# Optimization experiments

Hardware: AMD Instinct MI355X
Metric: run time of the kernel (lower is better)

## Reference

```python
import jax, jax.numpy as jnp
import numpy as np

B, N, M, D = 16, 1024, 4096, 256

def setup_inputs() -> dict:
    key = jax.random.key(0)
    k1, k2 = jax.random.split(key)
    encode = jax.random.normal(k1, (B, N, D), dtype=jnp.float32)
    # Codebook initialized uniform(-1/M, 1/M) in the torch module; use normal-scaled
    # values of comparable magnitude for a non-degenerate test.
    templat = jax.random.uniform(k2, (M, D), dtype=jnp.float32, minval=-1.0 / M, maxval=1.0 / M)
    return {"encode": encode, "templat": templat}

def reference(encode, templat):
    # eval-mode forward: match(encode, sample=False), detach='encode'
    enc = jax.lax.stop_gradient(encode)
    # squared-L2 distance via the expansion used in the source
    # dist[b,n,m] = |e|^2 - 2 e.t + |t|^2
    e_sq = jnp.sum(enc * enc, axis=-1, keepdims=True)        # (B,N,1)
    t_sq = jnp.sum(templat * templat, axis=-1)                # (M,)
    cross = jnp.einsum('bnd,md->bnm', enc, templat)           # (B,N,M)
    logits = -(e_sq - 2.0 * cross + t_sq)                     # (B,N,M)
    # zsoft = softmax(logits) computed in the module but only zidx/quant returned
    zidx = jnp.argmax(logits, axis=-1)                        # (B,N) int
    quant = templat[zidx]                                     # (B,N,D) gather
    return quant, zidx
```

## Files before the change

### kernel.cpp

```cpp
#include <hip/hip_runtime.h>


typedef _Float16 half8 __attribute__((ext_vector_type(8)));
typedef float f32x4 __attribute__((ext_vector_type(4)));

constexpr int B_ = 16, N_ = 1024, M_ = 4096, D_ = 256;
constexpr int ROWS = B_ * N_;
constexpr int BR = 128;
constexpr int BC = 128;
constexpr int NCT = 4;
constexpr int CS = 8;
constexpr int CPB = BC * NCT;
constexpr int KC = 32;
constexpr int LDH = 40;
constexpr int NPART = CS * 2;
constexpr float TSCALE = 131072.0f;
constexpr float INV2 = 1.52587890625e-05f;

__global__ void split_kernel(const float* __restrict__ E, const float* __restrict__ T,
                             _Float16* __restrict__ Ehi, _Float16* __restrict__ Elo,
                             _Float16* __restrict__ Thi, _Float16* __restrict__ Tlo) {
    int idx = blockIdx.x * blockDim.x + threadIdx.x;
    int row = idx >> 5;
    int c8 = (idx & 31) * 8;
    if (row >= ROWS + M_) return;
    const float* src;
    _Float16 *hi, *lo;
    size_t off;
    float scale;
    if (row < ROWS) {
        off = (size_t)row * D_ + c8;
        src = E + off; hi = Ehi; lo = Elo; scale = 1.0f;
    } else {
        off = (size_t)(row - ROWS) * D_ + c8;
        src = T + off; hi = Thi; lo = Tlo; scale = TSCALE;
    }
    float x[8];
    *reinterpret_cast<float4*>(&x[0]) = *reinterpret_cast<const float4*>(src);
    *reinterpret_cast<float4*>(&x[4]) = *reinterpret_cast<const float4*>(src + 4);
    half8 h, l;
    #pragma unroll
    for (int j = 0; j < 8; j++) {
        float xs = x[j] * scale;
        _Float16 hh = (_Float16)xs;
        h[j] = hh;
        l[j] = (_Float16)(xs - (float)hh);
    }
    *reinterpret_cast<half8*>(hi + off) = h;
    *reinterpret_cast<half8*>(lo + off) = l;
}

__global__ void rowsq_kernel(const float* __restrict__ E, const float* __restrict__ T,
                             float* __restrict__ esq, float* __restrict__ tsq) {
    int gt = blockIdx.x * blockDim.x + threadIdx.x;
    int row = gt >> 4;
    int l = gt & 15;
    if (row >= ROWS + M_) return;
    const float* src = (row < ROWS) ? (E + (size_t)row * D_)
                                    : (T + (size_t)(row - ROWS) * D_);
    const float* p = src + (l >> 3) * 128 + (l & 7);
    float r = __fmul_rn(p[0], p[0]);
    #pragma unroll
    for (int i = 1; i < 16; i++) {
        float x = p[8 * i];
        r = __fadd_rn(r, __fmul_rn(x, x));
    }
    float u = __fadd_rn(r, __shfl_xor(r, 1, 64));
    float v = __fadd_rn(u, __shfl_xor(u, 2, 64));
    float w = __fadd_rn(v, __shfl_xor(v, 4, 64));
    float s = __fadd_rn(w, __shfl_xor(w, 8, 64));
    if (l == 0) {
        if (row < ROWS) esq[row] = s;
        else            tsq[row - ROWS] = s;
    }
}

__global__ __launch_bounds__(256) void score_kernel(
    const _Float16* __restrict__ Ehi_g, const _Float16* __restrict__ Elo_g,
    const _Float16* __restrict__ Thi_g, const _Float16* __restrict__ Tlo_g,
    const float* __restrict__ esq, const float* __restrict__ tsq,
    float2* __restrict__ part) {
    __shared__ _Float16 Ehi[BR][LDH];
    __shared__ _Float16 Elo[BR][LDH];
    __shared__ _Float16 Thi[BC][LDH];
    __shared__ _Float16 Tlo[BC][LDH];

    const int tid = threadIdx.x;
    const int w  = tid >> 6;
    const int l  = tid & 63;
    const int wr = w >> 1;
    const int wc = w & 1;
    const int q  = l >> 4;
    const int cl = l & 15;
    const int row0 = blockIdx.x * BR;
    const int cs = blockIdx.y;
    const int colB = cs * CPB;

    const int srow  = tid >> 1;
    const int skoff = (tid & 1) * 16;

    float er[16];
    #pragma unroll
    for (int fr = 0; fr < 4; fr++)
        #pragma unroll
        for (int rg = 0; rg < 4; rg++)
            er[fr * 4 + rg] = esq[row0 + wr * 64 + fr * 16 + q * 4 + rg];

    float best[16];
    int   bidx[16];
    #pragma unroll
    for (int i = 0; i < 16; i++) { best[i] = 3.4e38f; bidx[i] = 0; }

    for (int ct = 0; ct < NCT; ct++) {
        const int col0 = colB + ct * BC;
        f32x4 acc[4][4];
        #pragma unroll
        for (int i = 0; i < 4; i++)
            #pragma unroll
            for (int j = 0; j < 4; j++)
                acc[i][j] = (f32x4){0.f, 0.f, 0.f, 0.f};

        for (int kc = 0; kc < D_; kc += KC) {
            __syncthreads();
            {
                const size_t eo = (size_t)(row0 + srow) * D_ + kc + skoff;
                half8 eh0 = *reinterpret_cast<const half8*>(Ehi_g + eo);
                half8 eh1 = *reinterpret_cast<const half8*>(Ehi_g + eo + 8);
                half8 el0 = *reinterpret_cast<const half8*>(Elo_g + eo);
                half8 el1 = *reinterpret_cast<const half8*>(Elo_g + eo + 8);
                const size_t to = (size_t)(col0 + srow) * D_ + kc + skoff;
                half8 th0 = *reinterpret_cast<const half8*>(Thi_g + to);
                half8 th1 = *reinterpret_cast<const half8*>(Thi_g + to + 8);
                half8 tl0 = *reinterpret_cast<const half8*>(Tlo_g + to);
                half8 tl1 = *reinterpret_cast<const half8*>(Tlo_g + to + 8);
                *reinterpret_cast<half8*>(&Ehi[srow][skoff])     = eh0;
                *reinterpret_cast<half8*>(&Ehi[srow][skoff + 8]) = eh1;
                *reinterpret_cast<half8*>(&Elo[srow][skoff])     = el0;
                *reinterpret_cast<half8*>(&Elo[srow][skoff + 8]) = el1;
                *reinterpret_cast<half8*>(&Thi[srow][skoff])     = th0;
                *reinterpret_cast<half8*>(&Thi[srow][skoff + 8]) = th1;
                *reinterpret_cast<half8*>(&Tlo[srow][skoff])     = tl0;
                *reinterpret_cast<half8*>(&Tlo[srow][skoff + 8]) = tl1;
            }
            __syncthreads();

            half8 ah[4], bh[4], tmp[4];
            #pragma unroll
            for (int f = 0; f < 4; f++)
                ah[f] = *reinterpret_cast<const half8*>(&Ehi[wr * 64 + f * 16 + cl][q * 8]);
            #pragma unroll
            for (int f = 0; f < 4; f++)
                bh[f] = *reinterpret_cast<const half8*>(&Thi[wc * 64 + f * 16 + cl][q * 8]);
            #pragma unroll
            for (int i = 0; i < 4; i++)
                #pragma unroll
                for (int j = 0; j < 4; j++)
                    acc[i][j] = __builtin_amdgcn_mfma_f32_16x16x32_f16(ah[i], bh[j], acc[i][j], 0, 0, 0);
            #pragma unroll
            for (int f = 0; f < 4; f++)
                tmp[f] = *reinterpret_cast<const half8*>(&Tlo[wc * 64 + f * 16 + cl][q * 8]);
            #pragma unroll
            for (int i = 0; i < 4; i++)
                #pragma unroll
                for (int j = 0; j < 4; j++)
                    acc[i][j] = __builtin_amdgcn_mfma_f32_16x16x32_f16(ah[i], tmp[j], acc[i][j], 0, 0, 0);
            #pragma unroll
            for (int f = 0; f < 4; f++)
                tmp[f] = *reinterpret_cast<const half8*>(&Elo[wr * 64 + f * 16 + cl][q * 8]);
            #pragma unroll
            for (int i = 0; i < 4; i++)
                #pragma unroll
                for (int j = 0; j < 4; j++)
                    acc[i][j] = __builtin_amdgcn_mfma_f32_16x16x32_f16(tmp[i], bh[j], acc[i][j], 0, 0, 0);
        }

        #pragma unroll
        for (int fc = 0; fc < 4; fc++) {
            const int col = col0 + wc * 64 + fc * 16 + cl;
            const float tc = tsq[col];
            #pragma unroll
            for (int fr = 0; fr < 4; fr++)
                #pragma unroll
                for (int rg = 0; rg < 4; rg++) {
                    const float c2 = acc[fr][fc][rg] * INV2;
                    const float d1 = __fsub_rn(er[fr * 4 + rg], c2);
                    const float d2 = __fadd_rn(d1, tc);
                    const int s = fr * 4 + rg;
                    if (d2 < best[s]) { best[s] = d2; bidx[s] = col; }
                }
        }
    }

    #pragma unroll
    for (int s = 0; s < 16; s++) {
        float v = best[s]; int i = bidx[s];
        #pragma unroll
        for (int off = 1; off < 16; off <<= 1) {
            float ov = __shfl_xor(v, off, 64);
            int   oi = __shfl_xor(i, off, 64);
            if (ov < v || (ov == v && oi < i)) { v = ov; i = oi; }
        }
        if (cl == 0) {
            const int row = row0 + wr * 64 + (s >> 2) * 16 + q * 4 + (s & 3);
            part[(size_t)row * NPART + cs * 2 + wc] = make_float2(v, __int_as_float(i));
        }
    }
}

__global__ void gather_kernel(const float* __restrict__ T, const float2* __restrict__ part,
                              float* __restrict__ quant, float* __restrict__ zout) {
    int gt = blockIdx.x * blockDim.x + threadIdx.x;
    int w = gt >> 6, lane = gt & 63;
    if (w >= ROWS) return;
    float2 p = part[(size_t)w * NPART];
    float v = p.x; int idx = __float_as_int(p.y);
    #pragma unroll
    for (int c = 1; c < NPART; c++) {
        float2 q = part[(size_t)w * NPART + c];
        int qi = __float_as_int(q.y);
        if (q.x < v || (q.x == v && qi < idx)) { v = q.x; idx = qi; }
    }
    float4 t = *reinterpret_cast<const float4*>(T + (size_t)idx * D_ + lane * 4);
    *reinterpret_cast<float4*>(quant + (size_t)w * D_ + lane * 4) = t;
    if (lane == 0) zout[w] = (float)idx;
}

extern "C" void kernel_launch(void* const* d_in, const int* in_sizes, int n_in,
                              void* d_out, int out_size, void* d_ws, size_t ws_size,
                              hipStream_t stream) {
    const float* E = (const float*)d_in[0];
    const float* T = (const float*)d_in[1];
    float* quant = (float*)d_out;
    float* zout  = quant + (size_t)ROWS * D_;

    float* esq   = (float*)d_ws;
    float* tsq   = esq + ROWS;
    float2* part = (float2*)(tsq + M_);
    _Float16* Ehi = (_Float16*)(part + (size_t)ROWS * NPART);
    _Float16* Elo = Ehi + (size_t)ROWS * D_;
    _Float16* Thi = Elo + (size_t)ROWS * D_;
    _Float16* Tlo = Thi + (size_t)M_ * D_;

    hipLaunchKernelGGL(split_kernel, dim3((ROWS + M_) * 32 / 256), dim3(256), 0, stream,
                       E, T, Ehi, Elo, Thi, Tlo);
    hipLaunchKernelGGL(rowsq_kernel, dim3((ROWS + M_) * 16 / 256), dim3(256), 0, stream, E, T, esq, tsq);
    hipLaunchKernelGGL(score_kernel, dim3(ROWS / BR, CS), dim3(256), 0, stream,
                       Ehi, Elo, Thi, Tlo, esq, tsq, part);
    hipLaunchKernelGGL(gather_kernel, dim3(ROWS * 64 / 256), dim3(256), 0, stream, T, part, quant, zout);
}
```

Measured before the change: 154.6 us.

## Double-buffer LDS tiles with register prefetch and flatten chunk loop

Flattens the column-tile and K-chunk loops into a single loop over chunks and double-buffers the shared-memory tiles. The next chunk's global loads are issued into registers right after the barrier so they overlap the MFMA work, which also removes one barrier per chunk. LDS row padding changes from 40 to 36 halves, so LDS accesses are split into 8-byte pieces to keep them aligned, which likely targets bank conflicts. The costs are doubled LDS, extra live registers for the prefetch and more, narrower LDS instructions.

```diff
diff --git a/kernel.cpp b/kernel.cpp
--- a/kernel.cpp
+++ b/kernel.cpp
@@ -1,6 +1,7 @@
 #include <hip/hip_runtime.h>
 
 
+typedef _Float16 half4 __attribute__((ext_vector_type(4)));
 typedef _Float16 half8 __attribute__((ext_vector_type(8)));
 typedef float f32x4 __attribute__((ext_vector_type(4)));
 
@@ -12,10 +13,23 @@
 constexpr int CS = 8;
 constexpr int CPB = BC * NCT;
 constexpr int KC = 32;
-constexpr int LDH = 40;
+constexpr int NCH = NCT * (D_ / KC);
+constexpr int LDH = 36;
 constexpr int NPART = CS * 2;
 constexpr float TSCALE = 131072.0f;
 constexpr float INV2 = 1.52587890625e-05f;
+
+__device__ inline void st8(_Float16* p, half8 v) {
+    half4 a = {v[0], v[1], v[2], v[3]};
+    half4 b = {v[4], v[5], v[6], v[7]};
+    *reinterpret_cast<half4*>(p) = a;
+    *reinterpret_cast<half4*>(p + 4) = b;
+}
+__device__ inline half8 ld8(const _Float16* p) {
+    half4 a = *reinterpret_cast<const half4*>(p);
+    half4 b = *reinterpret_cast<const half4*>(p + 4);
+    return (half8){a[0], a[1], a[2], a[3], b[0], b[1], b[2], b[3]};
+}
 
 __global__ void split_kernel(const float* __restrict__ E, const float* __restrict__ T,
                              _Float16* __restrict__ Ehi, _Float16* __restrict__ Elo,
@@ -80,10 +94,10 @@
     const _Float16* __restrict__ Thi_g, const _Float16* __restrict__ Tlo_g,
     const float* __restrict__ esq, const float* __restrict__ tsq,
     float2* __restrict__ part) {
-    __shared__ _Float16 Ehi[BR][LDH];
-    __shared__ _Float16 Elo[BR][LDH];
-    __shared__ _Float16 Thi[BC][LDH];
-    __shared__ _Float16 Tlo[BC][LDH];
+    __shared__ _Float16 Eh[2][BR][LDH];
+    __shared__ _Float16 El[2][BR][LDH];
+    __shared__ _Float16 Th[2][BC][LDH];
+    __shared__ _Float16 Tl[2][BC][LDH];
 
     const int tid = threadIdx.x;
     const int w  = tid >> 6;
@@ -111,84 +125,90 @@
     #pragma unroll
     for (int i = 0; i < 16; i++) { best[i] = 3.4e38f; bidx[i] = 0; }
 
-    for (int ct = 0; ct < NCT; ct++) {
-        const int col0 = colB + ct * BC;
-        f32x4 acc[4][4];
-        #pragma unroll
-        for (int i = 0; i < 4; i++)
-            #pragma unroll
-            for (int j = 0; j < 4; j++)
-                acc[i][j] = (f32x4){0.f, 0.f, 0.f, 0.f};
-
-        for (int kc = 0; kc < D_; kc += KC) {
-            __syncthreads();
-            {
-                const size_t eo = (size_t)(row0 + srow) * D_ + kc + skoff;
-                half8 eh0 = *reinterpret_cast<const half8*>(Ehi_g + eo);
-                half8 eh1 = *reinterpret_cast<const half8*>(Ehi_g + eo + 8);
-                half8 el0 = *reinterpret_cast<const half8*>(Elo_g + eo);
-                half8 el1 = *reinterpret_cast<const half8*>(Elo_g + eo + 8);
-                const size_t to = (size_t)(col0 + srow) * D_ + kc + skoff;
-                half8 th0 = *reinterpret_cast<const half8*>(Thi_g + to);
-                half8 th1 = *reinterpret_cast<const half8*>(Thi_g + to + 8);
-                half8 tl0 = *reinterpret_cast<const half8*>(Tlo_g + to);
-                half8 tl1 = *reinterpret_cast<const half8*>(Tlo_g + to + 8);
-                *reinterpret_cast<half8*>(&Ehi[srow][skoff])     = eh0;
-                *reinterpret_cast<half8*>(&Ehi[srow][skoff + 8]) = eh1;
-                *reinterpret_cast<half8*>(&Elo[srow][skoff])     = el0;
-                *reinterpret_cast<half8*>(&Elo[srow][skoff + 8]) = el1;
-                *reinterpret_cast<half8*>(&Thi[srow][skoff])     = th0;
-                *reinterpret_cast<half8*>(&Thi[srow][skoff + 8]) = th1;
-                *reinterpret_cast<half8*>(&Tlo[srow][skoff])     = tl0;
-                *reinterpret_cast<half8*>(&Tlo[srow][skoff + 8]) = tl1;
-            }
-            __syncthreads();
-
-            half8 ah[4], bh[4], tmp[4];
-            #pragma unroll
-            for (int f = 0; f < 4; f++)
-                ah[f] = *reinterpret_cast<const half8*>(&Ehi[wr * 64 + f * 16 + cl][q * 8]);
-            #pragma unroll
-            for (int f = 0; f < 4; f++)
-                bh[f] = *reinterpret_cast<const half8*>(&Thi[wc * 64 + f * 16 + cl][q * 8]);
+    half8 rE0, rE1, rF0, rF1, rG0, rG1, rH0, rH1;
+    const size_t eo_base = (size_t)(row0 + srow) * D_ + skoff;
+    #define LOADREGS(ch)                                                        \
+        {                                                                       \
+            const int ct_ = (ch) >> 3, kc_ = ((ch) & 7) * KC;                   \
+            const size_t eo = eo_base + kc_;                                    \
+            const size_t to = (size_t)(colB + ct_ * BC + srow) * D_ + kc_ + skoff; \
+            rE0 = *reinterpret_cast<const half8*>(Ehi_g + eo);                  \
+            rE1 = *reinterpret_cast<const half8*>(Ehi_g + eo + 8);              \
+            rF0 = *reinterpret_cast<const half8*>(Elo_g + eo);                  \
+            rF1 = *reinterpret_cast<const half8*>(Elo_g + eo + 8);              \
+            rG0 = *reinterpret_cast<const half8*>(Thi_g + to);                  \
+            rG1 = *reinterpret_cast<const half8*>(Thi_g + to + 8);              \
+            rH0 = *reinterpret_cast<const half8*>(Tlo_g + to);                  \
+            rH1 = *reinterpret_cast<const half8*>(Tlo_g + to + 8);              \
+        }
+
+    LOADREGS(0);
+    f32x4 acc[4][4];
+    int buf = 0;
+
+    for (int ch = 0; ch < NCH; ++ch) {
+        if ((ch & 7) == 0) {
             #pragma unroll
             for (int i = 0; i < 4; i++)
                 #pragma unroll
                 for (int j = 0; j < 4; j++)
-                    acc[i][j] = __builtin_amdgcn_mfma_f32_16x16x32_f16(ah[i], bh[j], acc[i][j], 0, 0, 0);
-            #pragma unroll
-            for (int f = 0; f < 4; f++)
-                tmp[f] = *reinterpret_cast<const half8*>(&Tlo[wc * 64 + f * 16 + cl][q * 8]);
-            #pragma unroll
-            for (int i = 0; i < 4; i++)
+                    acc[i][j] = (f32x4){0.f, 0.f, 0.f, 0.f};
+        }
+        st8(&Eh[buf][srow][skoff], rE0); st8(&Eh[buf][srow][skoff + 8], rE1);
+        st8(&El[buf][srow][skoff], rF0); st8(&El[buf][srow][skoff + 8], rF1);
+        st8(&Th[buf][srow][skoff], rG0); st8(&Th[buf][srow][skoff + 8], rG1);
+        st8(&Tl[buf][srow][skoff], rH0); st8(&Tl[buf][srow][skoff + 8], rH1);
+        __syncthreads();
+        if (ch < NCH - 1) LOADREGS(ch + 1);
+
+        half8 ah[4], bh[4], tmp[4];
+        #pragma unroll
+        for (int f = 0; f < 4; f++)
+            ah[f] = ld8(&Eh[buf][wr * 64 + f * 16 + cl][q * 8]);
+        #pragma unroll
+        for (int f = 0; f < 4; f++)
+            bh[f] = ld8(&Th[buf][wc * 64 + f * 16 + cl][q * 8]);
+        #pragma unroll
+        for (int i = 0; i < 4; i++)
+            #pragma unroll
+            for (int j = 0; j < 4; j++)
+                acc[i][j] = __builtin_amdgcn_mfma_f32_16x16x32_f16(ah[i], bh[j], acc[i][j], 0, 0, 0);
+        #pragma unroll
+        for (int f = 0; f < 4; f++)
+            tmp[f] = ld8(&Tl[buf][wc * 64 + f * 16 + cl][q * 8]);
+        #pragma unroll
+        for (int i = 0; i < 4; i++)
+            #pragma unroll
+            for (int j = 0; j < 4; j++)
+                acc[i][j] = __builtin_amdgcn_mfma_f32_16x16x32_f16(ah[i], tmp[j], acc[i][j], 0, 0, 0);
+        #pragma unroll
+        for (int f = 0; f < 4; f++)
+            tmp[f] = ld8(&El[buf][wr * 64 + f * 16 + cl][q * 8]);
+        #pragma unroll
+        for (int i = 0; i < 4; i++)
+            #pragma unroll
+            for (int j = 0; j < 4; j++)
+                acc[i][j] = __builtin_amdgcn_mfma_f32_16x16x32_f16(tmp[i], bh[j], acc[i][j], 0, 0, 0);
+
+        if ((ch & 7) == 7) {
+            const int col0 = colB + (ch >> 3) * BC;
+            #pragma unroll
+            for (int fc = 0; fc < 4; fc++) {
+                const int col = col0 + wc * 64 + fc * 16 + cl;
+                const float tc = tsq[col];
                 #pragma unroll
-                for (int j = 0; j < 4; j++)
-                    acc[i][j] = __builtin_amdgcn_mfma_f32_16x16x32_f16(ah[i], tmp[j], acc[i][j], 0, 0, 0);
-            #pragma unroll
-            for (int f = 0; f < 4; f++)
-                tmp[f] = *reinterpret_cast<const half8*>(&Elo[wr * 64 + f * 16 + cl][q * 8]);
-            #pragma unroll
-            for (int i = 0; i < 4; i++)
-                #pragma unroll
-                for (int j = 0; j < 4; j++)
-                    acc[i][j] = __builtin_amdgcn_mfma_f32_16x16x32_f16(tmp[i], bh[j], acc[i][j], 0, 0, 0);
-        }
-
-        #pragma unroll
-        for (int fc = 0; fc < 4; fc++) {
-            const int col = col0 + wc * 64 + fc * 16 + cl;
-            const float tc = tsq[col];
-            #pragma unroll
-            for (int fr = 0; fr < 4; fr++)
-                #pragma unroll
-                for (int rg = 0; rg < 4; rg++) {
-                    const float c2 = acc[fr][fc][rg] * INV2;
-                    const float d1 = __fsub_rn(er[fr * 4 + rg], c2);
-                    const float d2 = __fadd_rn(d1, tc);
-                    const int s = fr * 4 + rg;
-                    if (d2 < best[s]) { best[s] = d2; bidx[s] = col; }
-                }
-        }
+                for (int fr = 0; fr < 4; fr++)
+                    #pragma unroll
+                    for (int rg = 0; rg < 4; rg++) {
+                        const float c2 = acc[fr][fc][rg] * INV2;
+                        const float d1 = __fsub_rn(er[fr * 4 + rg], c2);
+                        const float d2 = __fadd_rn(d1, tc);
+                        const int s = fr * 4 + rg;
+                        if (d2 < best[s]) { best[s] = d2; bidx[s] = col; }
+                    }
+            }
+        }
+        buf ^= 1;
     }
 
     #pragma unroll
```

After: 231.9 us. 1.5x slower.

## Stage score-kernel tiles with direct global-to-LDS loads and flatten chunk loop

Applied to the files above, without the earlier changes.

Replaces the register-staged global loads and LDS stores in the score kernel with global_load_lds direct-to-LDS transfers of 16 bytes per lane. The LDS row stride drops from 40 to 32 halves so each wave's rows are contiguous, as the intrinsic requires. The column-tile and k-chunk loops are merged into one flat loop, with accumulators reset and the argmin epilogue run at tile boundaries. This removes the VGPR round-trip and the separate ds_write instructions, but the unpadded stride may bring back LDS bank conflicts on the MFMA fragment reads, and there is still no double buffering.

```diff
diff --git a/kernel.cpp b/kernel.cpp
--- a/kernel.cpp
+++ b/kernel.cpp
@@ -12,10 +12,17 @@
 constexpr int CS = 8;
 constexpr int CPB = BC * NCT;
 constexpr int KC = 32;
-constexpr int LDH = 40;
+constexpr int NCH = NCT * (D_ / KC);
+constexpr int LDH = 32;
 constexpr int NPART = CS * 2;
 constexpr float TSCALE = 131072.0f;
 constexpr float INV2 = 1.52587890625e-05f;
+
+__device__ __forceinline__ void gload16(const _Float16* g, _Float16* l) {
+    __builtin_amdgcn_global_load_lds(
+        (const __attribute__((address_space(1))) void*)g,
+        (__attribute__((address_space(3))) void*)l, 16, 0, 0);
+}
 
 __global__ void split_kernel(const float* __restrict__ E, const float* __restrict__ T,
                              _Float16* __restrict__ Ehi, _Float16* __restrict__ Elo,
@@ -80,10 +87,10 @@
     const _Float16* __restrict__ Thi_g, const _Float16* __restrict__ Tlo_g,
     const float* __restrict__ esq, const float* __restrict__ tsq,
     float2* __restrict__ part) {
-    __shared__ _Float16 Ehi[BR][LDH];
-    __shared__ _Float16 Elo[BR][LDH];
-    __shared__ _Float16 Thi[BC][LDH];
-    __shared__ _Float16 Tlo[BC][LDH];
+    __shared__ _Float16 Eh[BR][LDH];
+    __shared__ _Float16 El[BR][LDH];
+    __shared__ _Float16 Th[BC][LDH];
+    __shared__ _Float16 Tl[BC][LDH];
 
     const int tid = threadIdx.x;
     const int w  = tid >> 6;
@@ -96,8 +103,8 @@
     const int cs = blockIdx.y;
     const int colB = cs * CPB;
 
-    const int srow  = tid >> 1;
-    const int skoff = (tid & 1) * 16;
+    const int lrow = l >> 2;
+    const int lk   = (l & 3) * 8;
 
     float er[16];
     #pragma unroll
@@ -111,83 +118,83 @@
     #pragma unroll
     for (int i = 0; i < 16; i++) { best[i] = 3.4e38f; bidx[i] = 0; }
 
-    for (int ct = 0; ct < NCT; ct++) {
-        const int col0 = colB + ct * BC;
-        f32x4 acc[4][4];
-        #pragma unroll
-        for (int i = 0; i < 4; i++)
-            #pragma unroll
-            for (int j = 0; j < 4; j++)
-                acc[i][j] = (f32x4){0.f, 0.f, 0.f, 0.f};
-
-        for (int kc = 0; kc < D_; kc += KC) {
-            __syncthreads();
-            {
-                const size_t eo = (size_t)(row0 + srow) * D_ + kc + skoff;
-                half8 eh0 = *reinterpret_cast<const half8*>(Ehi_g + eo);
-                half8 eh1 = *reinterpret_cast<const half8*>(Ehi_g + eo + 8);
-                half8 el0 = *reinterpret_cast<const half8*>(Elo_g + eo);
-                half8 el1 = *reinterpret_cast<const half8*>(Elo_g + eo + 8);
-                const size_t to = (size_t)(col0 + srow) * D_ + kc + skoff;
-                half8 th0 = *reinterpret_cast<const half8*>(Thi_g + to);
-                half8 th1 = *reinterpret_cast<const half8*>(Thi_g + to + 8);
-                half8 tl0 = *reinterpret_cast<const half8*>(Tlo_g + to);
-                half8 tl1 = *reinterpret_cast<const half8*>(Tlo_g + to + 8);
-                *reinterpret_cast<half8*>(&Ehi[srow][skoff])     = eh0;
-                *reinterpret_cast<half8*>(&Ehi[srow][skoff + 8]) = eh1;
-                *reinterpret_cast<half8*>(&Elo[srow][skoff])     = el0;
-                *reinterpret_cast<half8*>(&Elo[srow][skoff + 8]) = el1;
-                *reinterpret_cast<half8*>(&Thi[srow][skoff])     = th0;
-                *reinterpret_cast<half8*>(&Thi[srow][skoff + 8]) = th1;
-                *reinterpret_cast<half8*>(&Tlo[srow][skoff])     = tl0;
-                *reinterpret_cast<half8*>(&Tlo[srow][skoff + 8]) = tl1;
-            }
-            __syncthreads();
-
-            half8 ah[4], bh[4], tmp[4];
-            #pragma unroll
-            for (int f = 0; f < 4; f++)
-                ah[f] = *reinterpret_cast<const half8*>(&Ehi[wr * 64 + f * 16 + cl][q * 8]);
-            #pragma unroll
-            for (int f = 0; f < 4; f++)
-                bh[f] = *reinterpret_cast<const half8*>(&Thi[wc * 64 + f * 16 + cl][q * 8]);
+    f32x4 acc[4][4];
+
+    for (int ch = 0; ch < NCH; ++ch) {
+        const int ct = ch >> 3;
+        const int kc = (ch & 7) * KC;
+        if ((ch & 7) == 0) {
             #pragma unroll
             for (int i = 0; i < 4; i++)
                 #pragma unroll
                 for (int j = 0; j < 4; j++)
-                    acc[i][j] = __builtin_amdgcn_mfma_f32_16x16x32_f16(ah[i], bh[j], acc[i][j], 0, 0, 0);
-            #pragma unroll
-            for (int f = 0; f < 4; f++)
-                tmp[f] = *reinterpret_cast<const half8*>(&Tlo[wc * 64 + f * 16 + cl][q * 8]);
-            #pragma unroll
-            for (int i = 0; i < 4; i++)
+                    acc[i][j] = (f32x4){0.f, 0.f, 0.f, 0.f};
+        }
+        __syncthreads();
+        {
+            const size_t eb = (size_t)(row0 + 32 * w) * D_ + kc + lk;
+            const size_t tb = (size_t)(colB + ct * BC + 32 * w) * D_ + kc + lk;
+            #pragma unroll
+            for (int i = 0; i < 2; i++) {
+                const size_t go = (size_t)(16 * i + lrow) * D_;
+                _Float16* ldsE = &Eh[32 * w + 16 * i][0];
+                _Float16* ldsF = &El[32 * w + 16 * i][0];
+                _Float16* ldsG = &Th[32 * w + 16 * i][0];
+                _Float16* ldsH = &Tl[32 * w + 16 * i][0];
+                gload16(Ehi_g + eb + go, ldsE);
+                gload16(Elo_g + eb + go, ldsF);
+                gload16(Thi_g + tb + go, ldsG);
+                gload16(Tlo_g + tb + go, ldsH);
+            }
+        }
+        __syncthreads();
+
+        half8 ah[4], bh[4], tmp[4];
+        #pragma unroll
+        for (int f = 0; f < 4; f++)
+            ah[f] = *reinterpret_cast<const half8*>(&Eh[wr * 64 + f * 16 + cl][q * 8]);
+        #pragma unroll
+        for (int f = 0; f < 4; f++)
+            bh[f] = *reinterpret_cast<const half8*>(&Th[wc * 64 + f * 16 + cl][q * 8]);
+        #pragma unroll
+        for (int i = 0; i < 4; i++)
+            #pragma unroll
+            for (int j = 0; j < 4; j++)
+                acc[i][j] = __builtin_amdgcn_mfma_f32_16x16x32_f16(ah[i], bh[j], acc[i][j], 0, 0, 0);
+        #pragma unroll
+        for (int f = 0; f < 4; f++)
+            tmp[f] = *reinterpret_cast<const half8*>(&Tl[wc * 64 + f * 16 + cl][q * 8]);
+        #pragma unroll
+        for (int i = 0; i < 4; i++)
+            #pragma unroll
+            for (int j = 0; j < 4; j++)
+                acc[i][j] = __builtin_amdgcn_mfma_f32_16x16x32_f16(ah[i], tmp[j], acc[i][j], 0, 0, 0);
+        #pragma unroll
+        for (int f = 0; f < 4; f++)
+            tmp[f] = *reinterpret_cast<const half8*>(&El[wr * 64 + f * 16 + cl][q * 8]);
+        #pragma unroll
+        for (int i = 0; i < 4; i++)
+            #pragma unroll
+            for (int j = 0; j < 4; j++)
+                acc[i][j] = __builtin_amdgcn_mfma_f32_16x16x32_f16(tmp[i], bh[j], acc[i][j], 0, 0, 0);
+
+        if ((ch & 7) == 7) {
+            const int col0 = colB + ct * BC;
+            #pragma unroll
+            for (int fc = 0; fc < 4; fc++) {
+                const int col = col0 + wc * 64 + fc * 16 + cl;
+                const float tc = tsq[col];
                 #pragma unroll
-                for (int j = 0; j < 4; j++)
-                    acc[i][j] = __builtin_amdgcn_mfma_f32_16x16x32_f16(ah[i], tmp[j], acc[i][j], 0, 0, 0);
-            #pragma unroll
-            for (int f = 0; f < 4; f++)
-                tmp[f] = *reinterpret_cast<const half8*>(&Elo[wr * 64 + f * 16 + cl][q * 8]);
-            #pragma unroll
-            for (int i = 0; i < 4; i++)
-                #pragma unroll
-                for (int j = 0; j < 4; j++)
-                    acc[i][j] = __builtin_amdgcn_mfma_f32_16x16x32_f16(tmp[i], bh[j], acc[i][j], 0, 0, 0);
-        }
-
-        #pragma unroll
-        for (int fc = 0; fc < 4; fc++) {
-            const int col = col0 + wc * 64 + fc * 16 + cl;
-            const float tc = tsq[col];
-            #pragma unroll
-            for (int fr = 0; fr < 4; fr++)
-                #pragma unroll
-                for (int rg = 0; rg < 4; rg++) {
-                    const float c2 = acc[fr][fc][rg] * INV2;
-                    const float d1 = __fsub_rn(er[fr * 4 + rg], c2);
-                    const float d2 = __fadd_rn(d1, tc);
-                    const int s = fr * 4 + rg;
-                    if (d2 < best[s]) { best[s] = d2; bidx[s] = col; }
-                }
+                for (int fr = 0; fr < 4; fr++)
+                    #pragma unroll
+                    for (int rg = 0; rg < 4; rg++) {
+                        const float c2 = acc[fr][fc][rg] * INV2;
+                        const float d1 = __fsub_rn(er[fr * 4 + rg], c2);
+                        const float d2 = __fadd_rn(d1, tc);
+                        const int s = fr * 4 + rg;
+                        if (d2 < best[s]) { best[s] = d2; bidx[s] = col; }
+                    }
+            }
         }
     }
 
```

After: 238.5 us. +54.3%, slower.
